# Kernel tuning notes

Measured on AMD Instinct MI355X. Metric: run time of the kernel, lower is better.

Reference implementation:

```python
import jax, jax.numpy as jnp
import numpy as np

B, N, M, K = 4, 2048, 8192, 3          # batches, coarse pts/batch, fine pts/batch, knn k
C_IN, C_SKIP, H, C_OUT = 256, 128, 256, 128


def setup_inputs() -> dict:
    key = jax.random.key(0)
    ks = jax.random.split(key, 8)
    x = jax.random.normal(ks[0], (B * N, C_IN), jnp.float32)
    pos = jax.random.normal(ks[1], (B * N, 3), jnp.float32)
    batch = jnp.repeat(jnp.arange(B, dtype=jnp.int64), N)        # sorted, equal-sized batches
    x_skip = jax.random.normal(ks[2], (B * M, C_SKIP), jnp.float32)
    pos_skip = jax.random.normal(ks[3], (B * M, 3), jnp.float32)
    batch_skip = jnp.repeat(jnp.arange(B, dtype=jnp.int64), M)
    # MLP params: Linear(384->256) + ReLU + Linear(256->128)
    W1 = jax.random.normal(ks[4], (C_IN + C_SKIP, H), jnp.float32) / np.sqrt(C_IN + C_SKIP)
    b1 = jnp.zeros((H,), jnp.float32)
    W2 = jax.random.normal(ks[5], (H, C_OUT), jnp.float32) / np.sqrt(H)
    b2 = jnp.zeros((C_OUT,), jnp.float32)
    return {"x": x, "pos": pos, "x_skip": x_skip, "pos_skip": pos_skip,
            "W1": W1, "b1": b1, "W2": W2, "b2": b2,
            "batch": batch, "batch_skip": batch_skip}


def _knn_interpolate(x, pos, pos_skip):
    # x: [B*N, C], pos: [B*N, 3], pos_skip: [B*M, 3]; batches are equal-sized & sorted,
    # so per-batch kNN == reshape to [B, n, ...] (matches batch/batch_skip vectors).
    xb = x.reshape(B, N, C_IN)
    pb = pos.reshape(B, N, 3)
    qb = pos_skip.reshape(B, M, 3)
    # squared pairwise distances via GEMM expansion: [B, M, N]
    d2 = (jnp.sum(qb * qb, -1)[:, :, None]
          + jnp.sum(pb * pb, -1)[:, None, :]
          - 2.0 * jnp.einsum('bmd,bnd->bmn', qb, pb))
    neg_d2, idx = jax.lax.top_k(-d2, K)           # k smallest distances
    d2k = jnp.maximum(-neg_d2, 0.0)               # [B, M, K]
    w = 1.0 / (d2k + 1e-16)                       # inverse-squared-distance weights
    feats = xb[jnp.arange(B)[:, None, None], idx] # gather: [B, M, K, C]
    interp = jnp.sum(w[..., None] * feats, axis=2) / jnp.sum(w, axis=2)[..., None]
    return interp.reshape(B * M, C_IN)


def reference(x, pos, x_skip, pos_skip, W1, b1, W2, b2, batch, batch_skip):
    xi = _knn_interpolate(x, pos, pos_skip)              # [B*M, C_IN]
    h = jnp.concatenate([xi, x_skip], axis=1)            # [B*M, C_IN+C_SKIP]
    h = jax.nn.relu(h @ W1 + b1)
    out = h @ W2 + b2                                    # [B*M, C_OUT]
    return (out, pos_skip, batch_skip)
```

## Files before the change

kernel.cpp:

```cpp
#include <hip/hip_runtime.h>
#include <math.h>
#include <stdint.h>

#define Bn    4
#define Nn    2048
#define Mn    8192
#define CIN   256
#define CSKIP 128
#define HID   256
#define COUT  128
#define KTOT  384

typedef short bf16x8 __attribute__((ext_vector_type(8)));
typedef float f32x16 __attribute__((ext_vector_type(16)));

__device__ __forceinline__ ushort f2bf(float f) {
    union { float f; unsigned u; } v; v.f = f;
    return (ushort)((v.u + 0x7fffu + ((v.u >> 16) & 1u)) >> 16);
}

__global__ __launch_bounds__(256) void convert_kernel(
    const float* __restrict__ xs, const float* __restrict__ W1,
    const float* __restrict__ W2, ushort* __restrict__ Abig,
    ushort* __restrict__ W1T, ushort* __restrict__ W2T)
{
    const int bid = blockIdx.x, tid = threadIdx.x;
    if (bid < 4096) {
        const int q   = bid * 256 + tid;
        const int row = q >> 5;
        const int cq  = (q & 31) * 4;
        const float4 v = *(const float4*)(xs + (size_t)row * CSKIP + cq);
        ushort4 o; o.x = f2bf(v.x); o.y = f2bf(v.y); o.z = f2bf(v.z); o.w = f2bf(v.w);
        *(ushort4*)(Abig + (size_t)row * KTOT + CIN + cq) = o;
    } else if (bid < 4096 + 96) {
        const int q  = (bid - 4096) * 256 + tid;
        const int n  = q / 96;
        const int kq = (q % 96) * 4;
        ushort4 o;
        o.x = f2bf(W1[(size_t)(kq + 0) * HID + n]);
        o.y = f2bf(W1[(size_t)(kq + 1) * HID + n]);
        o.z = f2bf(W1[(size_t)(kq + 2) * HID + n]);
        o.w = f2bf(W1[(size_t)(kq + 3) * HID + n]);
        *(ushort4*)(W1T + (size_t)n * KTOT + kq) = o;
    } else {
        const int q  = (bid - 4192) * 256 + tid;
        const int n  = q >> 6;
        const int kq = (q & 63) * 4;
        ushort4 o;
        o.x = f2bf(W2[(size_t)(kq + 0) * COUT + n]);
        o.y = f2bf(W2[(size_t)(kq + 1) * COUT + n]);
        o.z = f2bf(W2[(size_t)(kq + 2) * COUT + n]);
        o.w = f2bf(W2[(size_t)(kq + 3) * COUT + n]);
        *(ushort4*)(W2T + (size_t)n * HID + kq) = o;
    }
}

__global__ __launch_bounds__(256) void knn_interp_kernel(
    const float* __restrict__ x,
    const float* __restrict__ pos,
    const float* __restrict__ pos_skip,
    ushort* __restrict__ Abig)
{
    __shared__ float4 spos[Nn];
    __shared__ float  sPd[32][8][3];
    __shared__ int    sPi[32][8][3];
    __shared__ int    sIdx[32][3];
    __shared__ float  sW[32][4];

    const int tid    = threadIdx.x;
    const int qloc   = tid & 31;
    const int chunk  = tid >> 5;
    const int blockQ = blockIdx.x * 32;
    const int b      = blockQ / Mn;

    for (int i = tid; i < Nn; i += 256) {
        const float* p = pos + (size_t)(b * Nn + i) * 3;
        float p0 = p[0], p1 = p[1], p2 = p[2];
        float pp = __fadd_rn(__fadd_rn(__fmul_rn(p0, p0), __fmul_rn(p1, p1)),
                             __fmul_rn(p2, p2));
        spos[i] = make_float4(p0, p1, p2, pp);
    }
    __syncthreads();

    const int q = blockQ + qloc;
    const float* qp = pos_skip + (size_t)q * 3;
    const float q0 = qp[0], q1 = qp[1], q2 = qp[2];
    const float qq = __fadd_rn(__fadd_rn(__fmul_rn(q0, q0), __fmul_rn(q1, q1)),
                               __fmul_rn(q2, q2));

    float dA = INFINITY, dB = INFINITY, dC = INFINITY;
    int   iA = 0, iB = 0, iC = 0;
    const int base = chunk * 256;
#pragma unroll 4
    for (int j = 0; j < 256; ++j) {
        float4 P = spos[base + j];
        float dot = __fadd_rn(__fadd_rn(__fmul_rn(q0, P.x), __fmul_rn(q1, P.y)),
                              __fmul_rn(q2, P.z));
        float d = __fsub_rn(__fadd_rn(qq, P.w), __fmul_rn(2.0f, dot));
        if (d < dC) {
            if (d < dB) {
                dC = dB; iC = iB;
                if (d < dA) { dB = dA; iB = iA; dA = d; iA = base + j; }
                else        { dB = d;  iB = base + j; }
            } else { dC = d; iC = base + j; }
        }
    }
    sPd[qloc][chunk][0] = dA; sPd[qloc][chunk][1] = dB; sPd[qloc][chunk][2] = dC;
    sPi[qloc][chunk][0] = iA; sPi[qloc][chunk][1] = iB; sPi[qloc][chunk][2] = iC;
    __syncthreads();

    if (tid < 32) {
        float mA = INFINITY, mB = INFINITY, mC = INFINITY;
        int   jA = 0, jB = 0, jC = 0;
#pragma unroll
        for (int c = 0; c < 8; ++c) {
#pragma unroll
            for (int s = 0; s < 3; ++s) {
                float d = sPd[tid][c][s];
                int   i = sPi[tid][c][s];
                if (d < mC) {
                    if (d < mB) {
                        mC = mB; jC = jB;
                        if (d < mA) { mB = mA; jB = jA; mA = d; jA = i; }
                        else        { mB = d;  jB = i; }
                    } else { mC = d; jC = i; }
                }
            }
        }
        float w0 = 1.0f / (fmaxf(mA, 0.0f) + 1e-16f);
        float w1 = 1.0f / (fmaxf(mB, 0.0f) + 1e-16f);
        float w2 = 1.0f / (fmaxf(mC, 0.0f) + 1e-16f);
        sIdx[tid][0] = jA; sIdx[tid][1] = jB; sIdx[tid][2] = jC;
        sW[tid][0] = w0; sW[tid][1] = w1; sW[tid][2] = w2;
        sW[tid][3] = w0 + w1 + w2;
    }
    __syncthreads();

    const int wave = tid >> 6, lane = tid & 63;
    const size_t xbase = (size_t)b * Nn * CIN;
    for (int j = 0; j < 8; ++j) {
        const int lq = wave * 8 + j;
        const int gq = blockQ + lq;
        const int i0 = sIdx[lq][0], i1 = sIdx[lq][1], i2 = sIdx[lq][2];
        const float w0 = sW[lq][0], w1 = sW[lq][1], w2 = sW[lq][2], den = sW[lq][3];
        const float4 f0 = ((const float4*)(x + xbase + (size_t)i0 * CIN))[lane];
        const float4 f1 = ((const float4*)(x + xbase + (size_t)i1 * CIN))[lane];
        const float4 f2 = ((const float4*)(x + xbase + (size_t)i2 * CIN))[lane];
        ushort4 ov;
        ov.x = f2bf((w0 * f0.x + w1 * f1.x + w2 * f2.x) / den);
        ov.y = f2bf((w0 * f0.y + w1 * f1.y + w2 * f2.y) / den);
        ov.z = f2bf((w0 * f0.z + w1 * f1.z + w2 * f2.z) / den);
        ov.w = f2bf((w0 * f0.w + w1 * f1.w + w2 * f2.w) / den);
        *(ushort4*)(Abig + (size_t)gq * KTOT + lane * 4) = ov;
    }
}

__global__ __launch_bounds__(256, 1) void mlp_fused(
    const ushort* __restrict__ Abig,
    const ushort* __restrict__ W1T,
    const float*  __restrict__ b1,
    const ushort* __restrict__ W2T,
    const float*  __restrict__ b2,
    float* __restrict__ out)
{
    __shared__ ushort Ast[128 * 32];
    __shared__ ushort Bst[128 * 32];
    __shared__ ushort Hs [128 * 128];

    const int tid  = threadIdx.x;
    const int wave = tid >> 6, lane = tid & 63;
    const int wr = wave >> 1, wc = wave & 1;
    const int l31 = lane & 31, kc0 = lane >> 5;
    const long rowbase = (long)blockIdx.x * 128;

    const int sr0 = tid >> 2;
    const int ss0 = tid & 3;
    const int ssw = (ss0 ^ (sr0 & 3));

    f32x16 acc2[2][2];
#pragma unroll
    for (int i = 0; i < 2; ++i)
#pragma unroll
        for (int j = 0; j < 2; ++j)
#pragma unroll
            for (int e = 0; e < 16; ++e) acc2[i][j][e] = 0.0f;

    for (int nh = 0; nh < 2; ++nh) {
        f32x16 acc1[2][2];
#pragma unroll
        for (int i = 0; i < 2; ++i)
#pragma unroll
            for (int j = 0; j < 2; ++j)
#pragma unroll
                for (int e = 0; e < 16; ++e) acc1[i][j][e] = 0.0f;

        const ushort* Ab = Abig + (size_t)rowbase * KTOT;
        const ushort* Wb = W1T + (size_t)(nh * 128) * KTOT;

        uint4 ra0, ra1, rb0, rb1;
        ra0 = *(const uint4*)(Ab + (size_t)sr0 * KTOT + ss0 * 8);
        ra1 = *(const uint4*)(Ab + (size_t)(sr0 + 64) * KTOT + ss0 * 8);
        rb0 = *(const uint4*)(Wb + (size_t)sr0 * KTOT + ss0 * 8);
        rb1 = *(const uint4*)(Wb + (size_t)(sr0 + 64) * KTOT + ss0 * 8);

        for (int t = 0; t < 12; ++t) {
            __syncthreads();
            *(uint4*)&Ast[sr0 * 32 + (ssw << 3)]        = ra0;
            *(uint4*)&Ast[(sr0 + 64) * 32 + (ssw << 3)] = ra1;
            *(uint4*)&Bst[sr0 * 32 + (ssw << 3)]        = rb0;
            *(uint4*)&Bst[(sr0 + 64) * 32 + (ssw << 3)] = rb1;
            __syncthreads();
            if (t < 11) {
                const int kt = (t + 1) * 32;
                ra0 = *(const uint4*)(Ab + (size_t)sr0 * KTOT + kt + ss0 * 8);
                ra1 = *(const uint4*)(Ab + (size_t)(sr0 + 64) * KTOT + kt + ss0 * 8);
                rb0 = *(const uint4*)(Wb + (size_t)sr0 * KTOT + kt + ss0 * 8);
                rb1 = *(const uint4*)(Wb + (size_t)(sr0 + 64) * KTOT + kt + ss0 * 8);
            }
#pragma unroll
            for (int s = 0; s < 2; ++s) {
                bf16x8 af[2], bq[2];
#pragma unroll
                for (int mf = 0; mf < 2; ++mf) {
                    const int r = wr * 64 + mf * 32 + l31;
                    af[mf] = *(const bf16x8*)&Ast[r * 32 + ((((s << 1) | kc0) ^ (r & 3)) << 3)];
                }
#pragma unroll
                for (int nf = 0; nf < 2; ++nf) {
                    const int rn = wc * 64 + nf * 32 + l31;
                    bq[nf] = *(const bf16x8*)&Bst[rn * 32 + ((((s << 1) | kc0) ^ (rn & 3)) << 3)];
                }
#pragma unroll
                for (int mf = 0; mf < 2; ++mf)
#pragma unroll
                    for (int nf = 0; nf < 2; ++nf)
                        acc1[mf][nf] = __builtin_amdgcn_mfma_f32_32x32x16_bf16(
                            af[mf], bq[nf], acc1[mf][nf], 0, 0, 0);
            }
        }

#pragma unroll
        for (int mf = 0; mf < 2; ++mf)
#pragma unroll
            for (int nf = 0; nf < 2; ++nf) {
                const int col = wc * 64 + nf * 32 + l31;
                const float b1v = b1[nh * 128 + col];
#pragma unroll
                for (int e = 0; e < 16; ++e) {
                    const int rl = wr * 64 + mf * 32 + (e & 3) + ((e >> 2) << 3) + (kc0 << 2);
                    const float hv = fmaxf(acc1[mf][nf][e] + b1v, 0.0f);
                    Hs[rl * 128 + (((col >> 3) ^ (rl & 7)) << 3) + (col & 7)] = f2bf(hv);
                }
            }
        __syncthreads();

        uint4 rw0, rw1;
        rw0 = *(const uint4*)(W2T + (size_t)sr0 * HID + nh * 128 + ss0 * 8);
        rw1 = *(const uint4*)(W2T + (size_t)(sr0 + 64) * HID + nh * 128 + ss0 * 8);

        for (int t = 0; t < 4; ++t) {
            __syncthreads();
            *(uint4*)&Bst[sr0 * 32 + (ssw << 3)]        = rw0;
            *(uint4*)&Bst[(sr0 + 64) * 32 + (ssw << 3)] = rw1;
            __syncthreads();
            if (t < 3) {
                const int kt = nh * 128 + (t + 1) * 32;
                rw0 = *(const uint4*)(W2T + (size_t)sr0 * HID + kt + ss0 * 8);
                rw1 = *(const uint4*)(W2T + (size_t)(sr0 + 64) * HID + kt + ss0 * 8);
            }
#pragma unroll
            for (int s = 0; s < 2; ++s) {
                bf16x8 af[2], bq[2];
#pragma unroll
                for (int mf = 0; mf < 2; ++mf) {
                    const int r  = wr * 64 + mf * 32 + l31;
                    const int kc = (t << 2) + (s << 1) + kc0;
                    af[mf] = *(const bf16x8*)&Hs[r * 128 + ((kc ^ (r & 7)) << 3)];
                }
#pragma unroll
                for (int nf = 0; nf < 2; ++nf) {
                    const int rn = wc * 64 + nf * 32 + l31;
                    bq[nf] = *(const bf16x8*)&Bst[rn * 32 + ((((s << 1) | kc0) ^ (rn & 3)) << 3)];
                }
#pragma unroll
                for (int mf = 0; mf < 2; ++mf)
#pragma unroll
                    for (int nf = 0; nf < 2; ++nf)
                        acc2[mf][nf] = __builtin_amdgcn_mfma_f32_32x32x16_bf16(
                            af[mf], bq[nf], acc2[mf][nf], 0, 0, 0);
            }
        }
        __syncthreads();
    }

#pragma unroll
    for (int mf = 0; mf < 2; ++mf)
#pragma unroll
        for (int nf = 0; nf < 2; ++nf) {
            const int col = wc * 64 + nf * 32 + l31;
            const float b2v = b2[col];
#pragma unroll
            for (int e = 0; e < 16; ++e) {
                const int rl = wr * 64 + mf * 32 + (e & 3) + ((e >> 2) << 3) + (kc0 << 2);
                out[(rowbase + rl) * COUT + col] = acc2[mf][nf][e] + b2v;
            }
        }
}

__global__ __launch_bounds__(256) void tail_kernel(
    const float* __restrict__ pos_skip, float* __restrict__ dst)
{
    const int i = blockIdx.x * 256 + threadIdx.x;
    const int nPos = Bn * Mn * 3;
    if (i < nPos) {
        dst[i] = pos_skip[i];
    } else {
        const int j = i - nPos;
        dst[nPos + j] = (float)(j >> 13);
    }
}

extern "C" void kernel_launch(void* const* d_in, const int* in_sizes, int n_in,
                              void* d_out, int out_size, void* d_ws, size_t ws_size,
                              hipStream_t stream)
{
    const float* x        = (const float*)d_in[0];
    const float* pos      = (const float*)d_in[1];
    const float* x_skip   = (const float*)d_in[2];
    const float* pos_skip = (const float*)d_in[3];
    const float* W1       = (const float*)d_in[4];
    const float* b1       = (const float*)d_in[5];
    const float* W2       = (const float*)d_in[6];
    const float* b2       = (const float*)d_in[7];

    float* out = (float*)d_out;

    ushort* Abig = (ushort*)d_ws;
    ushort* W1T  = (ushort*)((char*)d_ws + (size_t)Bn * Mn * KTOT * 2);
    ushort* W2T  = (ushort*)((char*)W1T + (size_t)HID * KTOT * 2);

    convert_kernel<<<dim3(4096 + 96 + 32), 256, 0, stream>>>(
        x_skip, W1, W2, Abig, W1T, W2T);

    knn_interp_kernel<<<dim3(Bn * Mn / 32), 256, 0, stream>>>(x, pos, pos_skip, Abig);

    mlp_fused<<<dim3(Bn * Mn / 128), 256, 0, stream>>>(
        Abig, W1T, b1, W2T, b2, out);

    tail_kernel<<<dim3(512), 256, 0, stream>>>(
        pos_skip, out + (size_t)Bn * Mn * COUT);
}
```

Measured before the change: 85.87 us.

## Fuse conversion, kNN and tail copy into one launch; branchless top-3

Merges the bf16 conversion kernel, the kNN interpolation kernel and the tail copy kernel into a single launch. Block ranges pick which job each block does, which removes two launches and lets the memory-bound conversion overlap with the compute-bound kNN search. The kNN inner loop pre-scales the stored positions by 2, swaps the nested branch insertion for a branchless select-based top-3 update, and raises the unroll factor. Partial results in shared memory are transposed and padded to avoid bank conflicts. The cost is that the kNN blocks all need the large shared position array, so conversion blocks launched with the same kernel carry that shared footprint and may reduce occupancy.

```diff
diff --git a/kernel.cpp b/kernel.cpp
--- a/kernel.cpp
+++ b/kernel.cpp
@@ -19,58 +19,66 @@
     return (ushort)((v.u + 0x7fffu + ((v.u >> 16) & 1u)) >> 16);
 }
 
-__global__ __launch_bounds__(256) void convert_kernel(
-    const float* __restrict__ xs, const float* __restrict__ W1,
-    const float* __restrict__ W2, ushort* __restrict__ Abig,
-    ushort* __restrict__ W1T, ushort* __restrict__ W2T)
-{
-    const int bid = blockIdx.x, tid = threadIdx.x;
-    if (bid < 4096) {
-        const int q   = bid * 256 + tid;
-        const int row = q >> 5;
-        const int cq  = (q & 31) * 4;
-        const float4 v = *(const float4*)(xs + (size_t)row * CSKIP + cq);
-        ushort4 o; o.x = f2bf(v.x); o.y = f2bf(v.y); o.z = f2bf(v.z); o.w = f2bf(v.w);
-        *(ushort4*)(Abig + (size_t)row * KTOT + CIN + cq) = o;
-    } else if (bid < 4096 + 96) {
-        const int q  = (bid - 4096) * 256 + tid;
-        const int n  = q / 96;
-        const int kq = (q % 96) * 4;
-        ushort4 o;
-        o.x = f2bf(W1[(size_t)(kq + 0) * HID + n]);
-        o.y = f2bf(W1[(size_t)(kq + 1) * HID + n]);
-        o.z = f2bf(W1[(size_t)(kq + 2) * HID + n]);
-        o.w = f2bf(W1[(size_t)(kq + 3) * HID + n]);
-        *(ushort4*)(W1T + (size_t)n * KTOT + kq) = o;
-    } else {
-        const int q  = (bid - 4192) * 256 + tid;
-        const int n  = q >> 6;
-        const int kq = (q & 63) * 4;
-        ushort4 o;
-        o.x = f2bf(W2[(size_t)(kq + 0) * COUT + n]);
-        o.y = f2bf(W2[(size_t)(kq + 1) * COUT + n]);
-        o.z = f2bf(W2[(size_t)(kq + 2) * COUT + n]);
-        o.w = f2bf(W2[(size_t)(kq + 3) * COUT + n]);
-        *(ushort4*)(W2T + (size_t)n * HID + kq) = o;
-    }
-}
-
-__global__ __launch_bounds__(256) void knn_interp_kernel(
+__global__ __launch_bounds__(256) void fused_front(
     const float* __restrict__ x,
     const float* __restrict__ pos,
+    const float* __restrict__ xs,
     const float* __restrict__ pos_skip,
-    ushort* __restrict__ Abig)
+    const float* __restrict__ W1, const float* __restrict__ W2,
+    ushort* __restrict__ Abig,
+    ushort* __restrict__ W1T, ushort* __restrict__ W2T,
+    float* __restrict__ tail_dst)
 {
     __shared__ float4 spos[Nn];
-    __shared__ float  sPd[32][8][3];
-    __shared__ int    sPi[32][8][3];
+    __shared__ float  sPd[8][3][33];
+    __shared__ int    sPi[8][3][33];
     __shared__ int    sIdx[32][3];
     __shared__ float  sW[32][4];
 
-    const int tid    = threadIdx.x;
+    const int bid = blockIdx.x;
+    const int tid = threadIdx.x;
+
+    if (bid >= 1024) {
+        const int cb = bid - 1024;
+        if (cb < 4096) {
+            const int q   = cb * 256 + tid;
+            const int row = q >> 5;
+            const int cq  = (q & 31) * 4;
+            const float4 v = *(const float4*)(xs + (size_t)row * CSKIP + cq);
+            ushort4 o; o.x = f2bf(v.x); o.y = f2bf(v.y); o.z = f2bf(v.z); o.w = f2bf(v.w);
+            *(ushort4*)(Abig + (size_t)row * KTOT + CIN + cq) = o;
+        } else if (cb < 4192) {
+            const int q  = (cb - 4096) * 256 + tid;
+            const int n  = q / 96;
+            const int kq = (q % 96) * 4;
+            ushort4 o;
+            o.x = f2bf(W1[(size_t)(kq + 0) * HID + n]);
+            o.y = f2bf(W1[(size_t)(kq + 1) * HID + n]);
+            o.z = f2bf(W1[(size_t)(kq + 2) * HID + n]);
+            o.w = f2bf(W1[(size_t)(kq + 3) * HID + n]);
+            *(ushort4*)(W1T + (size_t)n * KTOT + kq) = o;
+        } else if (cb < 4224) {
+            const int q  = (cb - 4192) * 256 + tid;
+            const int n  = q >> 6;
+            const int kq = (q & 63) * 4;
+            ushort4 o;
+            o.x = f2bf(W2[(size_t)(kq + 0) * COUT + n]);
+            o.y = f2bf(W2[(size_t)(kq + 1) * COUT + n]);
+            o.z = f2bf(W2[(size_t)(kq + 2) * COUT + n]);
+            o.w = f2bf(W2[(size_t)(kq + 3) * COUT + n]);
+            *(ushort4*)(W2T + (size_t)n * HID + kq) = o;
+        } else {
+            const int i = (cb - 4224) * 256 + tid;
+            const int nPos = Bn * Mn * 3;
+            if (i < nPos) tail_dst[i] = pos_skip[i];
+            else          tail_dst[i] = (float)((i - nPos) >> 13);
+        }
+        return;
+    }
+
     const int qloc   = tid & 31;
     const int chunk  = tid >> 5;
-    const int blockQ = blockIdx.x * 32;
+    const int blockQ = bid * 32;
     const int b      = blockQ / Mn;
 
     for (int i = tid; i < Nn; i += 256) {
@@ -78,7 +86,7 @@
         float p0 = p[0], p1 = p[1], p2 = p[2];
         float pp = __fadd_rn(__fadd_rn(__fmul_rn(p0, p0), __fmul_rn(p1, p1)),
                              __fmul_rn(p2, p2));
-        spos[i] = make_float4(p0, p1, p2, pp);
+        spos[i] = make_float4(2.0f * p0, 2.0f * p1, 2.0f * p2, pp);
     }
     __syncthreads();
 
@@ -91,22 +99,20 @@
     float dA = INFINITY, dB = INFINITY, dC = INFINITY;
     int   iA = 0, iB = 0, iC = 0;
     const int base = chunk * 256;
-#pragma unroll 4
+#pragma unroll 8
     for (int j = 0; j < 256; ++j) {
-        float4 P = spos[base + j];
-        float dot = __fadd_rn(__fadd_rn(__fmul_rn(q0, P.x), __fmul_rn(q1, P.y)),
-                              __fmul_rn(q2, P.z));
-        float d = __fsub_rn(__fadd_rn(qq, P.w), __fmul_rn(2.0f, dot));
-        if (d < dC) {
-            if (d < dB) {
-                dC = dB; iC = iB;
-                if (d < dA) { dB = dA; iB = iA; dA = d; iA = base + j; }
-                else        { dB = d;  iB = base + j; }
-            } else { dC = d; iC = base + j; }
-        }
-    }
-    sPd[qloc][chunk][0] = dA; sPd[qloc][chunk][1] = dB; sPd[qloc][chunk][2] = dC;
-    sPi[qloc][chunk][0] = iA; sPi[qloc][chunk][1] = iB; sPi[qloc][chunk][2] = iC;
+        const float4 P = spos[base + j];
+        const float dot2 = __fadd_rn(__fadd_rn(__fmul_rn(q0, P.x), __fmul_rn(q1, P.y)),
+                                     __fmul_rn(q2, P.z));
+        const float d = __fsub_rn(__fadd_rn(qq, P.w), dot2);
+        const int idx = base + j;
+        const bool c1 = d < dA, c2 = d < dB, c3 = d < dC;
+        dC = c3 ? (c2 ? dB : d) : dC;  iC = c3 ? (c2 ? iB : idx) : iC;
+        dB = c2 ? (c1 ? dA : d) : dB;  iB = c2 ? (c1 ? iA : idx) : iB;
+        dA = c1 ? d : dA;              iA = c1 ? idx : iA;
+    }
+    sPd[chunk][0][qloc] = dA; sPd[chunk][1][qloc] = dB; sPd[chunk][2][qloc] = dC;
+    sPi[chunk][0][qloc] = iA; sPi[chunk][1][qloc] = iB; sPi[chunk][2][qloc] = iC;
     __syncthreads();
 
     if (tid < 32) {
@@ -116,20 +122,17 @@
         for (int c = 0; c < 8; ++c) {
 #pragma unroll
             for (int s = 0; s < 3; ++s) {
-                float d = sPd[tid][c][s];
-                int   i = sPi[tid][c][s];
-                if (d < mC) {
-                    if (d < mB) {
-                        mC = mB; jC = jB;
-                        if (d < mA) { mB = mA; jB = jA; mA = d; jA = i; }
-                        else        { mB = d;  jB = i; }
-                    } else { mC = d; jC = i; }
-                }
-            }
-        }
-        float w0 = 1.0f / (fmaxf(mA, 0.0f) + 1e-16f);
-        float w1 = 1.0f / (fmaxf(mB, 0.0f) + 1e-16f);
-        float w2 = 1.0f / (fmaxf(mC, 0.0f) + 1e-16f);
+                const float d = sPd[c][s][tid];
+                const int   i = sPi[c][s][tid];
+                const bool c1 = d < mA, c2 = d < mB, c3 = d < mC;
+                mC = c3 ? (c2 ? mB : d) : mC;  jC = c3 ? (c2 ? jB : i) : jC;
+                mB = c2 ? (c1 ? mA : d) : mB;  jB = c2 ? (c1 ? jA : i) : jB;
+                mA = c1 ? d : mA;              jA = c1 ? i : jA;
+            }
+        }
+        const float w0 = 1.0f / (fmaxf(mA, 0.0f) + 1e-16f);
+        const float w1 = 1.0f / (fmaxf(mB, 0.0f) + 1e-16f);
+        const float w2 = 1.0f / (fmaxf(mC, 0.0f) + 1e-16f);
         sIdx[tid][0] = jA; sIdx[tid][1] = jB; sIdx[tid][2] = jC;
         sW[tid][0] = w0; sW[tid][1] = w1; sW[tid][2] = w2;
         sW[tid][3] = w0 + w1 + w2;
@@ -307,19 +310,6 @@
         }
 }
 
-__global__ __launch_bounds__(256) void tail_kernel(
-    const float* __restrict__ pos_skip, float* __restrict__ dst)
-{
-    const int i = blockIdx.x * 256 + threadIdx.x;
-    const int nPos = Bn * Mn * 3;
-    if (i < nPos) {
-        dst[i] = pos_skip[i];
-    } else {
-        const int j = i - nPos;
-        dst[nPos + j] = (float)(j >> 13);
-    }
-}
-
 extern "C" void kernel_launch(void* const* d_in, const int* in_sizes, int n_in,
                               void* d_out, int out_size, void* d_ws, size_t ws_size,
                               hipStream_t stream)
@@ -339,14 +329,10 @@
     ushort* W1T  = (ushort*)((char*)d_ws + (size_t)Bn * Mn * KTOT * 2);
     ushort* W2T  = (ushort*)((char*)W1T + (size_t)HID * KTOT * 2);
 
-    convert_kernel<<<dim3(4096 + 96 + 32), 256, 0, stream>>>(
-        x_skip, W1, W2, Abig, W1T, W2T);
-
-    knn_interp_kernel<<<dim3(Bn * Mn / 32), 256, 0, stream>>>(x, pos, pos_skip, Abig);
+    fused_front<<<dim3(1024 + 4224 + 512), 256, 0, stream>>>(
+        x, pos, x_skip, pos_skip, W1, W2, Abig, W1T, W2T,
+        out + (size_t)Bn * Mn * COUT);
 
     mlp_fused<<<dim3(Bn * Mn / 128), 256, 0, stream>>>(
         Abig, W1T, b1, W2T, b2, out);
-
-    tail_kernel<<<dim3(512), 256, 0, stream>>>(
-        pos_skip, out + (size_t)Bn * Mn * COUT);
 }
```

New measurement: 77.23 us. 1.11x faster.
